# Kernel optimization log

Hardware: AMD Instinct MI355X
Metric: run time of the kernel (lower is better)

## Reference

```python
import jax, jax.numpy as jnp
import numpy as np

B, S, H, NH = 2, 2048, 1024, 16
DK = H // NH


def setup_inputs() -> dict:
    key = jax.random.key(0)
    ks = jax.random.split(key, 11)
    sc = 1.0 / np.sqrt(H)
    return {
        "q": jax.random.normal(ks[0], (B, S, H), jnp.float32),
        "v": jax.random.normal(ks[1], (B, S, H), jnp.float32),
        "k": jax.random.normal(ks[2], (B, S, H), jnp.float32),
        "Wq": jax.random.normal(ks[3], (H, H), jnp.float32) * sc,
        "bq": jax.random.normal(ks[4], (H,), jnp.float32) * 0.01,
        "Wk": jax.random.normal(ks[5], (H, H), jnp.float32) * sc,
        "bk": jax.random.normal(ks[6], (H,), jnp.float32) * 0.01,
        "Wv": jax.random.normal(ks[7], (H, H), jnp.float32) * sc,
        "bv": jax.random.normal(ks[8], (H,), jnp.float32) * 0.01,
        "Wo": jax.random.normal(ks[9], (H, H), jnp.float32) * sc,
        "bo": jax.random.normal(ks[10], (H,), jnp.float32) * 0.01,
    }


def reference(q, v, k, Wq, bq, Wk, bk, Wv, bv, Wo, bo):
    b, s, h = q.shape
    # projections; torch Linear computes x @ W.T + b
    qh = (q @ Wq.T + bq).reshape(b, s, NH, DK).transpose(0, 2, 1, 3)  # [B,NH,S,DK]
    kh = (k @ Wk.T + bk).reshape(b, s, NH, DK).transpose(0, 2, 1, 3)
    vh = (v @ Wv.T + bv).reshape(b, s, NH, DK).transpose(0, 2, 1, 3)
    scores = jnp.einsum("bhqd,bhkd->bhqk", qh, kh) / jnp.sqrt(
        jnp.asarray(DK, qh.dtype))  # [B,NH,S,S]
    probs = jax.nn.softmax(scores, axis=-1)
    ctx = jnp.einsum("bhqk,bhkd->bhqd", probs, vh)  # [B,NH,S,DK]
    concat = ctx.transpose(0, 2, 1, 3).reshape(b, s, h)
    return concat @ Wo.T + bo
```

## Files before the change

### kernel.cpp

```cpp
#include <hip/hip_runtime.h>
#include <cstddef>
#include <cstdint>

typedef _Float16 f16x8 __attribute__((ext_vector_type(8)));
typedef _Float16 f16x4 __attribute__((ext_vector_type(4)));
typedef __fp16   h16x2 __attribute__((ext_vector_type(2)));
typedef float    f32x4 __attribute__((ext_vector_type(4)));
typedef float    f32x2 __attribute__((ext_vector_type(2)));

constexpr int B_  = 2;
constexpr int S_  = 2048;
constexpr int H_  = 1024;
constexpr int NH_ = 16;
constexpr int DK_ = 64;
constexpr int M_  = B_ * S_;
constexpr int K_  = H_;

constexpr float SOFF = 4.0f;

#define MFMA32(a, b, c) __builtin_amdgcn_mfma_f32_16x16x32_f16((a), (b), (c), 0, 0, 0)

__device__ __forceinline__ void glds16(const void* g, void* l) {
    __builtin_amdgcn_global_load_lds(
        (const __attribute__((address_space(1))) void*)g,
        (__attribute__((address_space(3))) void*)l, 16, 0, 0);
}

struct CvtArgs {
    const float* s[7];
    _Float16*    d[7];
};

__global__ __launch_bounds__(256) void cvt7(CvtArgs a)
{
    const int bid = blockIdx.x;
    int seg, blk;
    if (bid < 6144) { seg = bid >> 11;               blk = bid & 2047; }
    else            { seg = 3 + ((bid - 6144) >> 9); blk = (bid - 6144) & 511; }
    const int i = (blk * 256 + threadIdx.x) * 8;
    const float4 v0 = *reinterpret_cast<const float4*>(a.s[seg] + i);
    const float4 v1 = *reinterpret_cast<const float4*>(a.s[seg] + i + 4);
    f16x8 o;
    o[0] = (_Float16)v0.x; o[1] = (_Float16)v0.y;
    o[2] = (_Float16)v0.z; o[3] = (_Float16)v0.w;
    o[4] = (_Float16)v1.x; o[5] = (_Float16)v1.y;
    o[6] = (_Float16)v1.z; o[7] = (_Float16)v1.w;
    *reinterpret_cast<f16x8*>(a.d[seg] + i) = o;
}

struct QkvArgs {
    const _Float16* A[3];
    const _Float16* W[3];
    const float*    bias[3];
    _Float16* dstQ;
    _Float16* dstK;
    _Float16* dstV;
    float qscale;
};

__global__ __launch_bounds__(256) void gemm_qkv(QkvArgs args)
{
    constexpr int BM = 128, BN = 128, BK = 32;
    __shared__ __align__(16) _Float16 sm[8192];
    auto As = reinterpret_cast<_Float16(*)[BK]>(sm);
    auto Ws = reinterpret_cast<_Float16(*)[BK]>(sm + 4096);
    auto Tr = reinterpret_cast<_Float16(*)[64]>(sm);

    const int z = blockIdx.z;
    const _Float16* __restrict__ A = args.A[z];
    const _Float16* __restrict__ W = args.W[z];
    const float* __restrict__ bias = args.bias[z];

    const int t = threadIdx.x;
    const int w = t >> 6, lane = t & 63, quad = lane >> 4, l16 = lane & 15;
    const int m0 = blockIdx.y * BM;
    const int n0 = blockIdx.x * BN;
    const int wr = (w & 1) * 64, wc = (w >> 1) * 64;
    const int srow = lane >> 2, scol = (lane & 3) * 8;

    f32x4 acc[4][4];
#pragma unroll
    for (int i = 0; i < 4; ++i)
#pragma unroll
        for (int j = 0; j < 4; ++j) acc[i][j] = (f32x4){0.f, 0.f, 0.f, 0.f};

    for (int k0 = 0; k0 < K_; k0 += BK) {
        glds16(&A[(size_t)(m0 + w * 32 + srow) * K_ + k0 + scol], &As[w * 32][0]);
        glds16(&A[(size_t)(m0 + w * 32 + 16 + srow) * K_ + k0 + scol], &As[w * 32 + 16][0]);
        glds16(&W[(size_t)(n0 + w * 32 + srow) * K_ + k0 + scol], &Ws[w * 32][0]);
        glds16(&W[(size_t)(n0 + w * 32 + 16 + srow) * K_ + k0 + scol], &Ws[w * 32 + 16][0]);
        __syncthreads();

        f16x8 af[4], bf[4];
#pragma unroll
        for (int i = 0; i < 4; ++i)
            af[i] = *reinterpret_cast<const f16x8*>(&As[wr + i * 16 + l16][quad * 8]);
#pragma unroll
        for (int j = 0; j < 4; ++j)
            bf[j] = *reinterpret_cast<const f16x8*>(&Ws[wc + j * 16 + l16][quad * 8]);
#pragma unroll
        for (int i = 0; i < 4; ++i)
#pragma unroll
            for (int j = 0; j < 4; ++j)
                acc[i][j] = MFMA32(af[i], bf[j], acc[i][j]);
        __syncthreads();
    }

    const float scale = (z == 0) ? args.qscale : 1.0f;
    float bv[4];
#pragma unroll
    for (int j = 0; j < 4; ++j) bv[j] = bias[n0 + wc + j * 16 + l16];

    if (z == 2) {
#pragma unroll
        for (int i = 0; i < 4; ++i) {
            const int sb = m0 + wr + i * 16 + quad * 4;
            const int b = sb >> 11, s = sb & (S_ - 1);
            const int kt = s >> 4;
            const int w4 = kt & 3, tIdx = kt >> 2;
            const int p16 = tIdx >> 1, sub = tIdx & 1;
#pragma unroll
            for (int j = 0; j < 4; ++j) {
                const int d = wc + j * 16 + l16;
                const int h = blockIdx.x * 2 + (d >> 6);
                const int dt = (d & 63) >> 4;
                f16x4 ov;
#pragma unroll
                for (int r = 0; r < 4; ++r) ov[r] = (_Float16)(acc[i][j][r] + bv[j]);
                _Float16* base = args.dstV + ((size_t)b * NH_ + h) * 131072
                    + (size_t)(((w4 * 16 + p16) * 4 + dt) * 512 + sub * 256 + lane * 4);
                *reinterpret_cast<f16x4*>(base) = ov;
            }
        }
        return;
    }

    _Float16* dst = (z == 0) ? args.dstQ : args.dstK;
    const int b = m0 >> 11, s0 = m0 & (S_ - 1);
#pragma unroll
    for (int ch = 0; ch < 2; ++ch) {
        __syncthreads();
        if ((w >> 1) == ch) {
#pragma unroll
            for (int i = 0; i < 4; ++i)
#pragma unroll
                for (int j = 0; j < 4; ++j)
#pragma unroll
                    for (int r = 0; r < 4; ++r)
                        Tr[wr + i * 16 + quad * 4 + r][j * 16 + l16] =
                            (_Float16)((acc[i][j][r] + bv[j]) * scale);
        }
        __syncthreads();
        const int h = blockIdx.x * 2 + ch;
        _Float16* dbase = dst + ((size_t)(b * NH_ + h) * S_ + s0) * DK_;
#pragma unroll
        for (int p = 0; p < 4; ++p) {
            const int c = t + p * 256;
            *reinterpret_cast<f16x8*>(&dbase[c * 8]) =
                *reinterpret_cast<const f16x8*>(&Tr[c >> 3][(c & 7) * 8]);
        }
    }
}

__global__ __launch_bounds__(256) void gemm_out(
    const _Float16* __restrict__ A, const _Float16* __restrict__ W,
    const float* __restrict__ bias, float* __restrict__ out)
{
    constexpr int BM = 64, BN = 128, BK = 32;
    __shared__ _Float16 As[BM][BK];
    __shared__ _Float16 Ws[BN][BK];

    const int t = threadIdx.x;
    const int w = t >> 6, lane = t & 63, quad = lane >> 4, l16 = lane & 15;
    const int m0 = blockIdx.y * BM;
    const int n0 = blockIdx.x * BN;
    const int wc = w * 32;
    const int srow = lane >> 2, scol = (lane & 3) * 8;

    f32x4 acc[4][2];
#pragma unroll
    for (int i = 0; i < 4; ++i)
#pragma unroll
        for (int j = 0; j < 2; ++j) acc[i][j] = (f32x4){0.f, 0.f, 0.f, 0.f};

    for (int k0 = 0; k0 < K_; k0 += BK) {
        glds16(&A[(size_t)(m0 + w * 16 + srow) * K_ + k0 + scol], &As[w * 16][0]);
        glds16(&W[(size_t)(n0 + w * 32 + srow) * K_ + k0 + scol], &Ws[w * 32][0]);
        glds16(&W[(size_t)(n0 + w * 32 + 16 + srow) * K_ + k0 + scol], &Ws[w * 32 + 16][0]);
        __syncthreads();

        f16x8 af[4], bf[2];
#pragma unroll
        for (int i = 0; i < 4; ++i)
            af[i] = *reinterpret_cast<const f16x8*>(&As[i * 16 + l16][quad * 8]);
#pragma unroll
        for (int j = 0; j < 2; ++j)
            bf[j] = *reinterpret_cast<const f16x8*>(&Ws[wc + j * 16 + l16][quad * 8]);
#pragma unroll
        for (int i = 0; i < 4; ++i)
#pragma unroll
            for (int j = 0; j < 2; ++j)
                acc[i][j] = MFMA32(af[i], bf[j], acc[i][j]);
        __syncthreads();
    }

    float bvv[2];
#pragma unroll
    for (int j = 0; j < 2; ++j) bvv[j] = bias[n0 + wc + j * 16 + l16];

#pragma unroll
    for (int i = 0; i < 4; ++i)
#pragma unroll
        for (int j = 0; j < 2; ++j)
#pragma unroll
            for (int r = 0; r < 4; ++r)
                out[(size_t)(m0 + i * 16 + quad * 4 + r) * H_ +
                    n0 + wc + j * 16 + l16] = acc[i][j][r] + bvv[j];
}

__global__ __launch_bounds__(256) void attn_mfma(
    const _Float16* __restrict__ qh, const _Float16* __restrict__ kh,
    const _Float16* __restrict__ vfrag, _Float16* __restrict__ ctx)
{
    __shared__ float Ob[4][64][36];
    __shared__ float Ls[4][64];
    __shared__ float Linv[64];

    const int t = threadIdx.x;
    const int w = t >> 6, lane = t & 63, quad = lane >> 4, l16 = lane & 15;

    const int lin = blockIdx.x;
    const int xcd = lin & 7, slot = lin >> 3;
    const int bh = xcd + 8 * (slot >> 5);
    const int q0 = (slot & 31) * 64;

    const _Float16* qb = qh + (size_t)bh * S_ * DK_;
    const _Float16* kb = kh + (size_t)bh * S_ * DK_;
    const _Float16* vb = vfrag + (size_t)bh * 131072;

    f16x8 qf[4][2];
#pragma unroll
    for (int qt = 0; qt < 4; ++qt)
#pragma unroll
        for (int h2 = 0; h2 < 2; ++h2)
            qf[qt][h2] = *reinterpret_cast<const f16x8*>(
                &qb[(size_t)(q0 + qt * 16 + l16) * DK_ + h2 * 32 + quad * 8]);

    const f32x4 msoff = (f32x4){-SOFF, -SOFF, -SOFF, -SOFF};

    f32x4 o[4][4];
#pragma unroll
    for (int dt = 0; dt < 4; ++dt)
#pragma unroll
        for (int qt = 0; qt < 4; ++qt) o[dt][qt] = (f32x4){0.f, 0.f, 0.f, 0.f};
    f32x2 lp2[4];
#pragma unroll
    for (int qt = 0; qt < 4; ++qt) lp2[qt] = (f32x2){0.f, 0.f};

    const _Float16* kp = kb + (size_t)(w * 16 + l16) * DK_ + quad * 8;
    const _Float16* vp = vb + (size_t)w * 32768 + lane * 4;

    f32x4 scA[4], scB[4];
    {
        const f16x8 kA0 = *reinterpret_cast<const f16x8*>(kp);
        const f16x8 kA1 = *reinterpret_cast<const f16x8*>(kp + 32);
        const f16x8 kB0 = *reinterpret_cast<const f16x8*>(kp + 64 * DK_);
        const f16x8 kB1 = *reinterpret_cast<const f16x8*>(kp + 64 * DK_ + 32);
        kp += 128 * DK_;
#pragma unroll
        for (int qt = 0; qt < 4; ++qt) {
            f32x4 t0 = MFMA32(kA0, qf[qt][0], msoff);
            scA[qt] = MFMA32(kA1, qf[qt][1], t0);
            f32x4 t1 = MFMA32(kB0, qf[qt][0], msoff);
            scB[qt] = MFMA32(kB1, qf[qt][1], t1);
        }
    }

    for (int p = 0; p < 16; ++p) {
        const _Float16* nk = (p < 15) ? kp : (kp - 128 * DK_);
        const f16x8 nA0 = *reinterpret_cast<const f16x8*>(nk);
        const f16x8 nA1 = *reinterpret_cast<const f16x8*>(nk + 32);
        const f16x8 nB0 = *reinterpret_cast<const f16x8*>(nk + 64 * DK_);
        const f16x8 nB1 = *reinterpret_cast<const f16x8*>(nk + 64 * DK_ + 32);
        kp = nk + 128 * DK_;

        f16x8 vf8[4];
#pragma unroll
        for (int dt = 0; dt < 4; ++dt) {
            const f16x4 lo = *reinterpret_cast<const f16x4*>(vp + dt * 512);
            const f16x4 hi = *reinterpret_cast<const f16x4*>(vp + dt * 512 + 256);
            reinterpret_cast<f16x4*>(&vf8[dt])[0] = lo;
            reinterpret_cast<f16x4*>(&vf8[dt])[1] = hi;
        }
        vp += 2048;

        f16x8 pf8[4];
#pragma unroll
        for (int qt = 0; qt < 4; ++qt) {
            const float a0 = __builtin_amdgcn_exp2f(scA[qt][0]);
            const float a1 = __builtin_amdgcn_exp2f(scA[qt][1]);
            const float a2 = __builtin_amdgcn_exp2f(scA[qt][2]);
            const float a3 = __builtin_amdgcn_exp2f(scA[qt][3]);
            const float b0 = __builtin_amdgcn_exp2f(scB[qt][0]);
            const float b1 = __builtin_amdgcn_exp2f(scB[qt][1]);
            const float b2 = __builtin_amdgcn_exp2f(scB[qt][2]);
            const float b3 = __builtin_amdgcn_exp2f(scB[qt][3]);
            lp2[qt] += ((f32x2){a0, a1} + (f32x2){a2, a3}) +
                       ((f32x2){b0, b1} + (f32x2){b2, b3});
            h16x2* ph = reinterpret_cast<h16x2*>(&pf8[qt]);
            ph[0] = __builtin_amdgcn_cvt_pkrtz(a0, a1);
            ph[1] = __builtin_amdgcn_cvt_pkrtz(a2, a3);
            ph[2] = __builtin_amdgcn_cvt_pkrtz(b0, b1);
            ph[3] = __builtin_amdgcn_cvt_pkrtz(b2, b3);
        }

        __builtin_amdgcn_s_setprio(1);
#pragma unroll
        for (int qt = 0; qt < 4; ++qt) {
            f32x4 t0 = MFMA32(nA0, qf[qt][0], msoff);
            scA[qt] = MFMA32(nA1, qf[qt][1], t0);
            f32x4 t1 = MFMA32(nB0, qf[qt][0], msoff);
            scB[qt] = MFMA32(nB1, qf[qt][1], t1);
        }
#pragma unroll
        for (int dt = 0; dt < 4; ++dt)
#pragma unroll
            for (int qt = 0; qt < 4; ++qt)
                o[dt][qt] = MFMA32(vf8[dt], pf8[qt], o[dt][qt]);
        __builtin_amdgcn_s_setprio(0);
    }

#pragma unroll
    for (int qt = 0; qt < 4; ++qt) {
        float l = lp2[qt][0] + lp2[qt][1];
        l += __shfl_xor(l, 16);
        l += __shfl_xor(l, 32);
        if (quad == 0) Ls[w][qt * 16 + l16] = l;
    }
    __syncthreads();
    if (t < 64)
        Linv[t] = 1.f / (((Ls[0][t] + Ls[1][t]) + (Ls[2][t] + Ls[3][t])));

    const int b = bh >> 4, hh = bh & 15;
    const int dg = t & 3, qq = t >> 2;
#pragma unroll
    for (int ph = 0; ph < 2; ++ph) {
        __syncthreads();
#pragma unroll
        for (int dl = 0; dl < 2; ++dl) {
            const int dt = ph * 2 + dl;
#pragma unroll
            for (int qt = 0; qt < 4; ++qt)
                *reinterpret_cast<f32x4*>(
                    &Ob[w][qt * 16 + l16][dl * 16 + quad * 4]) = o[dt][qt];
        }
        __syncthreads();
        f32x4 s0 = (f32x4){0.f, 0.f, 0.f, 0.f};
        f32x4 s1 = (f32x4){0.f, 0.f, 0.f, 0.f};
#pragma unroll
        for (int ww = 0; ww < 4; ++ww) {
            s0 += *reinterpret_cast<const f32x4*>(&Ob[ww][qq][dg * 8]);
            s1 += *reinterpret_cast<const f32x4*>(&Ob[ww][qq][dg * 8 + 4]);
        }
        const float li = Linv[qq];
        f16x8 ov;
#pragma unroll
        for (int r = 0; r < 4; ++r) {
            ov[r]     = (_Float16)(s0[r] * li);
            ov[4 + r] = (_Float16)(s1[r] * li);
        }
        *reinterpret_cast<f16x8*>(
            &ctx[((size_t)b * S_ + q0 + qq) * H_ + hh * 64 + ph * 32 + dg * 8]) = ov;
    }
}

extern "C" void kernel_launch(void* const* d_in, const int* in_sizes, int n_in,
                              void* d_out, int out_size, void* d_ws,
                              size_t ws_size, hipStream_t stream)
{
    (void)in_sizes; (void)n_in; (void)out_size; (void)ws_size;
    const float* q  = (const float*)d_in[0];
    const float* v  = (const float*)d_in[1];
    const float* k  = (const float*)d_in[2];
    const float* Wq = (const float*)d_in[3];
    const float* bq = (const float*)d_in[4];
    const float* Wk = (const float*)d_in[5];
    const float* bk = (const float*)d_in[6];
    const float* Wv = (const float*)d_in[7];
    const float* bv = (const float*)d_in[8];
    const float* Wo = (const float*)d_in[9];
    const float* bo = (const float*)d_in[10];
    float* out = (float*)d_out;

    constexpr size_t NACT = (size_t)M_ * K_;
    constexpr size_t NW   = (size_t)H_ * H_;
    _Float16* p = (_Float16*)d_ws;
    _Float16* q16  = p;
    _Float16* k16  = p + NACT;
    _Float16* v16  = p + 2 * NACT;
    _Float16* w16q = p + 3 * NACT;
    _Float16* w16k = w16q + NW;
    _Float16* w16v = w16k + NW;
    _Float16* w16o = w16v + NW;
    _Float16* qhd  = w16o + NW;
    _Float16* khd  = qhd + NACT;
    _Float16* vfr  = khd + NACT;
    _Float16* ctx  = q16;

    CvtArgs ca;
    ca.s[0] = q;  ca.d[0] = q16;
    ca.s[1] = v;  ca.d[1] = v16;
    ca.s[2] = k;  ca.d[2] = k16;
    ca.s[3] = Wq; ca.d[3] = w16q;
    ca.s[4] = Wk; ca.d[4] = w16k;
    ca.s[5] = Wv; ca.d[5] = w16v;
    ca.s[6] = Wo; ca.d[6] = w16o;
    cvt7<<<dim3(8192), 256, 0, stream>>>(ca);

    QkvArgs ga;
    ga.A[0] = q16;  ga.W[0] = w16q; ga.bias[0] = bq;
    ga.A[1] = k16;  ga.W[1] = w16k; ga.bias[1] = bk;
    ga.A[2] = v16;  ga.W[2] = w16v; ga.bias[2] = bv;
    ga.dstQ = qhd;  ga.dstK = khd;  ga.dstV = vfr;
    ga.qscale = 0.125f * 1.4426950408889634f;

    gemm_qkv<<<dim3(H_ / 128, M_ / 128, 3), 256, 0, stream>>>(ga);

    attn_mfma<<<dim3(S_ / 64 * B_ * NH_), 256, 0, stream>>>(qhd, khd, vfr, ctx);

    gemm_out<<<dim3(H_ / 128, M_ / 64), 256, 0, stream>>>(ctx, w16o, bo, out);
}
```

Measured before the change: 228.9 us.

## Double QKV GEMM K-tile with XOR-swizzled LDS; interleave V layout for wide loads

The QKV projection GEMM now stages a 64-wide K slice per iteration, in an XOR-swizzled LDS layout meant to avoid bank conflicts. This halves the number of barrier pairs per output tile but doubles LDS use per block. The V projection epilogue now writes the two sub-halves interleaved, so the attention kernel can load each V fragment with one 16-byte load instead of two 8-byte loads. The attention inner loop also issues the PV MFMAs before the next QK MFMAs, which changes how their dependencies get scheduled.

```diff
diff --git a/kernel.cpp b/kernel.cpp
--- a/kernel.cpp
+++ b/kernel.cpp
@@ -60,10 +60,10 @@
 
 __global__ __launch_bounds__(256) void gemm_qkv(QkvArgs args)
 {
-    constexpr int BM = 128, BN = 128, BK = 32;
-    __shared__ __align__(16) _Float16 sm[8192];
-    auto As = reinterpret_cast<_Float16(*)[BK]>(sm);
-    auto Ws = reinterpret_cast<_Float16(*)[BK]>(sm + 4096);
+    constexpr int BM = 128, BN = 128, BK = 64;
+    __shared__ __align__(16) _Float16 sm[16384];
+    _Float16* As = sm;
+    _Float16* Ws = sm + 8192;
     auto Tr = reinterpret_cast<_Float16(*)[64]>(sm);
 
     const int z = blockIdx.z;
@@ -76,7 +76,11 @@
     const int m0 = blockIdx.y * BM;
     const int n0 = blockIdx.x * BN;
     const int wr = (w & 1) * 64, wc = (w >> 1) * 64;
-    const int srow = lane >> 2, scol = (lane & 3) * 8;
+
+    const int srow = lane >> 3;
+    const int scol = ((lane & 7) ^ srow) * 8;
+
+    const int rx = (l16 & 7) << 4;
 
     f32x4 acc[4][4];
 #pragma unroll
@@ -85,24 +89,36 @@
         for (int j = 0; j < 4; ++j) acc[i][j] = (f32x4){0.f, 0.f, 0.f, 0.f};
 
     for (int k0 = 0; k0 < K_; k0 += BK) {
-        glds16(&A[(size_t)(m0 + w * 32 + srow) * K_ + k0 + scol], &As[w * 32][0]);
-        glds16(&A[(size_t)(m0 + w * 32 + 16 + srow) * K_ + k0 + scol], &As[w * 32 + 16][0]);
-        glds16(&W[(size_t)(n0 + w * 32 + srow) * K_ + k0 + scol], &Ws[w * 32][0]);
-        glds16(&W[(size_t)(n0 + w * 32 + 16 + srow) * K_ + k0 + scol], &Ws[w * 32 + 16][0]);
-        __syncthreads();
-
-        f16x8 af[4], bf[4];
-#pragma unroll
-        for (int i = 0; i < 4; ++i)
-            af[i] = *reinterpret_cast<const f16x8*>(&As[wr + i * 16 + l16][quad * 8]);
-#pragma unroll
-        for (int j = 0; j < 4; ++j)
-            bf[j] = *reinterpret_cast<const f16x8*>(&Ws[wc + j * 16 + l16][quad * 8]);
-#pragma unroll
-        for (int i = 0; i < 4; ++i)
+#pragma unroll
+        for (int c = 0; c < 4; ++c) {
+            const int r0 = w * 32 + c * 8;
+            glds16(&A[(size_t)(m0 + r0 + srow) * K_ + k0 + scol],
+                   As + r0 * 64);
+            glds16(&W[(size_t)(n0 + r0 + srow) * K_ + k0 + scol],
+                   Ws + r0 * 64);
+        }
+        __syncthreads();
+
+#pragma unroll
+        for (int ks = 0; ks < 2; ++ks) {
+            const int off = (ks * 64 + quad * 16) ^ rx;
+            f16x8 af[4], bf[4];
+#pragma unroll
+            for (int i = 0; i < 4; ++i)
+                af[i] = *reinterpret_cast<const f16x8*>(
+                    reinterpret_cast<const char*>(As) +
+                    (wr + i * 16 + l16) * 128 + off);
 #pragma unroll
             for (int j = 0; j < 4; ++j)
-                acc[i][j] = MFMA32(af[i], bf[j], acc[i][j]);
+                bf[j] = *reinterpret_cast<const f16x8*>(
+                    reinterpret_cast<const char*>(Ws) +
+                    (wc + j * 16 + l16) * 128 + off);
+#pragma unroll
+            for (int i = 0; i < 4; ++i)
+#pragma unroll
+                for (int j = 0; j < 4; ++j)
+                    acc[i][j] = MFMA32(af[i], bf[j], acc[i][j]);
+        }
         __syncthreads();
     }
 
@@ -128,7 +144,7 @@
 #pragma unroll
                 for (int r = 0; r < 4; ++r) ov[r] = (_Float16)(acc[i][j][r] + bv[j]);
                 _Float16* base = args.dstV + ((size_t)b * NH_ + h) * 131072
-                    + (size_t)(((w4 * 16 + p16) * 4 + dt) * 512 + sub * 256 + lane * 4);
+                    + (size_t)(((w4 * 16 + p16) * 4 + dt) * 512 + lane * 8 + sub * 4);
                 *reinterpret_cast<f16x4*>(base) = ov;
             }
         }
@@ -258,7 +274,7 @@
     for (int qt = 0; qt < 4; ++qt) lp2[qt] = (f32x2){0.f, 0.f};
 
     const _Float16* kp = kb + (size_t)(w * 16 + l16) * DK_ + quad * 8;
-    const _Float16* vp = vb + (size_t)w * 32768 + lane * 4;
+    const _Float16* vp = vb + (size_t)w * 32768 + lane * 8;
 
     f32x4 scA[4], scB[4];
     {
@@ -286,12 +302,8 @@
 
         f16x8 vf8[4];
 #pragma unroll
-        for (int dt = 0; dt < 4; ++dt) {
-            const f16x4 lo = *reinterpret_cast<const f16x4*>(vp + dt * 512);
-            const f16x4 hi = *reinterpret_cast<const f16x4*>(vp + dt * 512 + 256);
-            reinterpret_cast<f16x4*>(&vf8[dt])[0] = lo;
-            reinterpret_cast<f16x4*>(&vf8[dt])[1] = hi;
-        }
+        for (int dt = 0; dt < 4; ++dt)
+            vf8[dt] = *reinterpret_cast<const f16x8*>(vp + dt * 512);
         vp += 2048;
 
         f16x8 pf8[4];
@@ -316,17 +328,17 @@
 
         __builtin_amdgcn_s_setprio(1);
 #pragma unroll
+        for (int dt = 0; dt < 4; ++dt)
+#pragma unroll
+            for (int qt = 0; qt < 4; ++qt)
+                o[dt][qt] = MFMA32(vf8[dt], pf8[qt], o[dt][qt]);
+#pragma unroll
         for (int qt = 0; qt < 4; ++qt) {
             f32x4 t0 = MFMA32(nA0, qf[qt][0], msoff);
             scA[qt] = MFMA32(nA1, qf[qt][1], t0);
             f32x4 t1 = MFMA32(nB0, qf[qt][0], msoff);
             scB[qt] = MFMA32(nB1, qf[qt][1], t1);
         }
-#pragma unroll
-        for (int dt = 0; dt < 4; ++dt)
-#pragma unroll
-            for (int qt = 0; qt < 4; ++qt)
-                o[dt][qt] = MFMA32(vf8[dt], pf8[qt], o[dt][qt]);
         __builtin_amdgcn_s_setprio(0);
     }
 
```

Result: no change. 228.5 us (-0.2%).
